# Optimization experiments

Measured on AMD Instinct MI355X. Metric: run time of the kernel, lower is better.

The kernel has to match this reference:

```python
import jax, jax.numpy as jnp
import numpy as np

EPS = 1e-12  # F.normalize eps


def _l2norm(v, axis=-1):
    # torch.nn.functional.normalize: x / max(||x||_2, eps)
    n = jnp.sqrt(jnp.sum(v * v, axis=axis, keepdims=True))
    return v / jnp.maximum(n, EPS)


def setup_inputs() -> dict:
    key = jax.random.key(0)
    ks = jax.random.split(key, 4)
    B, C, W, H, Z = 8, 256, 16, 16, 16
    N, P = W * H * Z, 64
    heads = 8
    import math
    std_w = 1.0 / math.sqrt(C)      # nn.Linear default-ish scale
    std_ef = 1.0 / math.sqrt(P)     # init_() uses last-dim
    return {
        "x": jax.random.normal(ks[0], (B, C, W, H, Z), dtype=jnp.float32),
        "W_sa": jax.random.uniform(ks[1], (4 * C, C), jnp.float32, -std_w, std_w),
        "EF": jax.random.uniform(ks[2], (N, P), jnp.float32, -std_ef, std_ef),
        "temp2_sa": jnp.ones((heads, 1, 1), jnp.float32),
        "W_sc": jax.random.uniform(ks[3], (4 * C, C), jnp.float32, -std_w, std_w),
        "temp_sc": jnp.ones((heads, 1, 1), jnp.float32),
    }


def _qkvv(xf, Wt, heads):
    # xf: (B, N, C); torch Linear(hidden, 4*hidden, bias=False): y = x @ W.T
    B, N, C = xf.shape
    d = C // heads
    y = xf @ Wt.T                                   # (B, N, 4C)
    y = y.reshape(B, N, 4, heads, d)
    y = jnp.transpose(y, (2, 0, 3, 1, 4))           # (4, B, h, N, d)
    return y[0], y[1], y[2], y[3]


def reference(x, W_sa, EF, temp2_sa, W_sc, temp_sc):
    B, C, W, H, Z = x.shape
    N = W * H * Z
    heads = temp_sc.shape[0]
    d = C // heads
    xf = jnp.transpose(x.reshape(B, C, N), (0, 2, 1))  # (B, N, C)

    # ---- Spatial (Linformer-style projected) attention ----
    q, k, _, v_sa = _qkvv(xf, W_sa, heads)            # each (B, h, N, d)
    q_t = jnp.swapaxes(q, -2, -1)                     # (B, h, d, N)
    k_t = jnp.swapaxes(k, -2, -1)
    v_t = jnp.swapaxes(v_sa, -2, -1)
    k_proj = jnp.einsum('bhdn,nk->bhdk', k_t, EF)     # (B, h, d, P)
    v_proj = jnp.einsum('bhdn,nk->bhdk', v_t, EF)
    q_n = _l2norm(q_t, axis=-1)                       # normalize over N
    attn_sa = jnp.einsum('bhdn,bhdk->bhnk', q_n, k_proj) * temp2_sa  # (B,h,N,P)
    attn_sa = jax.nn.softmax(attn_sa, axis=-1)        # dropout: eval mode (identity)
    x_sa = jnp.einsum('bhnk,bhdk->bhnd', attn_sa, v_proj)            # (B,h,N,d)
    # faithful to original: permute(0,3,1,2) then reshape(B,N,C)
    x_sa = jnp.transpose(x_sa, (0, 3, 1, 2)).reshape(B, N, C)

    # ---- Channel (cross-covariance) attention ----
    qc, kc, v_ca, _ = _qkvv(xf, W_sc, heads)          # (B, h, N, d)
    qc_t = _l2norm(jnp.swapaxes(qc, -2, -1), axis=-1) # (B, h, d, N), norm over N
    kc_t = _l2norm(jnp.swapaxes(kc, -2, -1), axis=-1)
    vc_t = jnp.swapaxes(v_ca, -2, -1)                 # (B, h, d, N)
    attn_ca = jnp.einsum('bhdn,bhen->bhde', qc_t, kc_t) * temp_sc    # (B,h,d,d)
    attn_ca = jax.nn.softmax(attn_ca, axis=-1)
    x_ca = jnp.einsum('bhde,bhen->bhdn', attn_ca, vc_t)              # (B,h,d,N)
    x_ca = jnp.transpose(x_ca, (0, 3, 1, 2)).reshape(B, N, C)        # (B,N,h,d)->(B,N,C)

    feat = x_ca + x_sa
    out = jnp.transpose(feat.reshape(B, W, H, Z, C), (0, 4, 1, 2, 3))
    return out
```

## Files before the change

### kernel.cpp

```cpp
#include <hip/hip_runtime.h>

typedef unsigned short u16;
typedef unsigned int   u32;

typedef __attribute__((ext_vector_type(4))) short short4v;
typedef __attribute__((ext_vector_type(8))) short bf16x8;
typedef __attribute__((ext_vector_type(4))) float f32x4;


__device__ __forceinline__ float bf2f(u16 u){
  union { u32 i; float f; } v; v.i = ((u32)u) << 16; return v.f;
}
__device__ __forceinline__ u16 f2bf(float f){
  u32 u = __float_as_uint(f);
  u32 r = u + 0x7FFFu + ((u >> 16) & 1u);
  return (u16)(r >> 16);
}

__device__ __forceinline__ void gload_lds16(const u16* g, u16* l){
  __builtin_amdgcn_global_load_lds((const __attribute__((address_space(1))) void*)g,
                                   (__attribute__((address_space(3))) void*)l,
                                   16, 0, 0);
}

__global__ void k_detect(const u16* __restrict__ x, u32* __restrict__ flag){
  __shared__ int cnt[256];
  const int t = threadIdx.x;
  int c = 0;
  #pragma unroll
  for(int i = 0; i < 4; i++){
    u16 v = x[t * 4 + i];
    int e = (v >> 7) & 0xFF;
    if(e >= 112 && e <= 134) c++;
  }
  cnt[t] = c;
  __syncthreads();
  for(int s = 128; s > 0; s >>= 1){
    if(t < s) cnt[t] += cnt[t + s];
    __syncthreads();
  }
  if(t == 0) *flag = (cnt[0] < 800) ? 1u : 0u;
}

__global__ __launch_bounds__(256) void k_conv_bf(const void* __restrict__ src,
                                                 u16* __restrict__ dst, int n,
                                                 const u32* __restrict__ flag){
  const int i0 = (blockIdx.x * 256 + threadIdx.x) * 8;
  if(i0 >= n) return;
  const bool isf32 = (*flag != 0);
  if(isf32){
    const float4 a = *(const float4*)((const float*)src + i0);
    const float4 b = *(const float4*)((const float*)src + i0 + 4);
    uint4 o;
    o.x = (u32)f2bf(a.x) | ((u32)f2bf(a.y) << 16);
    o.y = (u32)f2bf(a.z) | ((u32)f2bf(a.w) << 16);
    o.z = (u32)f2bf(b.x) | ((u32)f2bf(b.y) << 16);
    o.w = (u32)f2bf(b.z) | ((u32)f2bf(b.w) << 16);
    *(uint4*)(dst + i0) = o;
  } else {
    *(uint4*)(dst + i0) = *(const uint4*)((const u16*)src + i0);
  }
}

__global__ __launch_bounds__(256) void k_conv_f32(const void* __restrict__ src,
                                                  float* __restrict__ dst, int n,
                                                  const u32* __restrict__ flag){
  const int i0 = (blockIdx.x * 256 + threadIdx.x) * 4;
  if(i0 >= n) return;
  const bool isf32 = (*flag != 0);
  if(isf32){
    *(float4*)(dst + i0) = *(const float4*)((const float*)src + i0);
  } else {
    const uint2 a = *(const uint2*)((const u16*)src + i0);
    float4 o;
    o.x = bf2f((u16)(a.x & 0xFFFF)); o.y = bf2f((u16)(a.x >> 16));
    o.z = bf2f((u16)(a.y & 0xFFFF)); o.w = bf2f((u16)(a.y >> 16));
    *(float4*)(dst + i0) = o;
  }
}

__global__ __launch_bounds__(256) void k_conv_both(const void* __restrict__ src,
                                                   float* __restrict__ dstf,
                                                   u16* __restrict__ dstb, int n,
                                                   int nb,
                                                   const u32* __restrict__ flag){
  const int i0 = (blockIdx.x * 256 + threadIdx.x) * 4;
  if(i0 >= n) return;
  const bool isf32 = (*flag != 0);
  float4 o;
  if(isf32){
    o = *(const float4*)((const float*)src + i0);
  } else {
    const uint2 a = *(const uint2*)((const u16*)src + i0);
    o.x = bf2f((u16)(a.x & 0xFFFF)); o.y = bf2f((u16)(a.x >> 16));
    o.z = bf2f((u16)(a.y & 0xFFFF)); o.w = bf2f((u16)(a.y >> 16));
  }
  *(float4*)(dstf + i0) = o;
  if(i0 < nb){
    uint2 pk;
    pk.x = (u32)f2bf(o.x) | ((u32)f2bf(o.y) << 16);
    pk.y = (u32)f2bf(o.z) | ((u32)f2bf(o.w) << 16);
    *(uint2*)(dstb + i0) = pk;
  }
}

__global__ __launch_bounds__(256) void k_convT(const void* __restrict__ src,
                                               u16* __restrict__ xb,
                                               u16* __restrict__ xT,
                                               const u32* __restrict__ flag){
  __shared__ u16 T[64][72];
  const int t = threadIdx.x;
  const int n0 = blockIdx.x * 64, c0 = blockIdx.y * 64, b = blockIdx.z;
  const int cl = t >> 2, ns = (t & 3) * 16;
  const bool isf32 = (*flag != 0);
  const size_t srcoff = ((size_t)(b * 256 + c0 + cl)) * 4096 + n0 + ns;
  u16 e[16];
  if(isf32){
    const float* sp = (const float*)src + srcoff;
    #pragma unroll
    for(int i = 0; i < 4; i++){
      const float4 v = *(const float4*)(sp + i * 4);
      e[i*4+0] = f2bf(v.x); e[i*4+1] = f2bf(v.y);
      e[i*4+2] = f2bf(v.z); e[i*4+3] = f2bf(v.w);
    }
  } else {
    const u16* sp = (const u16*)src + srcoff;
    *(uint4*)&e[0] = *(const uint4*)sp;
    *(uint4*)&e[8] = *(const uint4*)(sp + 8);
  }
  u16* xbp = xb + srcoff;
  *(uint4*)xbp       = *(uint4*)&e[0];
  *(uint4*)(xbp + 8) = *(uint4*)&e[8];
  #pragma unroll
  for(int i = 0; i < 16; i++) T[ns + i][cl] = e[i];
  __syncthreads();
  const int nl = t >> 2, cs = (t & 3) * 16;
  u16* xtp = xT + ((size_t)b * 4096 + n0 + nl) * 256 + c0 + cs;
  *(uint4*)xtp       = *(const uint4*)&T[nl][cs];
  *(uint4*)(xtp + 8) = *(const uint4*)&T[nl][cs + 8];
}

__global__ __launch_bounds__(256) void k_conv_efT(const void* __restrict__ src,
                                                  u16* __restrict__ EFT,
                                                  const u32* __restrict__ flag){
  __shared__ u16 T[64][72];
  const int t = threadIdx.x;
  const int n0 = blockIdx.x * 64;
  const int nl = t >> 2, p0 = (t & 3) * 16;
  const bool isf32 = (*flag != 0);
  const size_t off = (size_t)(n0 + nl) * 64 + p0;
  u16 e[16];
  if(isf32){
    const float* sp = (const float*)src + off;
    #pragma unroll
    for(int i = 0; i < 4; i++){
      const float4 v = *(const float4*)(sp + i * 4);
      e[i*4+0] = f2bf(v.x); e[i*4+1] = f2bf(v.y);
      e[i*4+2] = f2bf(v.z); e[i*4+3] = f2bf(v.w);
    }
  } else {
    const u16* sp = (const u16*)src + off;
    *(uint4*)&e[0] = *(const uint4*)sp;
    *(uint4*)&e[8] = *(const uint4*)(sp + 8);
  }
  #pragma unroll
  for(int i = 0; i < 16; i++) T[p0 + i][nl] = e[i];
  __syncthreads();
  const int pr = t >> 2, nn = (t & 3) * 16;
  u16* dp = EFT + (size_t)pr * 4096 + n0 + nn;
  *(uint4*)dp       = *(const uint4*)&T[pr][nn];
  *(uint4*)(dp + 8) = *(const uint4*)&T[pr][nn + 8];
}

__global__ __launch_bounds__(256) void k_qkv(const u16* __restrict__ Wc,
                                             const u16* __restrict__ xT,
                                             u16* __restrict__ Y){
  __shared__ union {
    struct { u16 Ws[128][64]; u16 Xs[128][64]; } s;
    u16 Cs[128][136];
  } L;
  const int t = threadIdx.x;
  const int n0 = blockIdx.x * 128, m0 = blockIdx.y * 128, b = blockIdx.z;
  const int w = t >> 6, lane = t & 63;
  const int fm = lane & 15, fq = lane >> 4;
  const int wm = w >> 1, wn = w & 1;
  const int lr = lane >> 3, lc = (lane & 7) * 8;
  const u16* gw = Wc + (size_t)m0 * 256;
  const u16* gx = xT + ((size_t)b * 4096 + n0) * 256;
  f32x4 acc[4][4] = {};
  for(int kc = 0; kc < 256; kc += 64){
    #pragma unroll
    for(int i = 0; i < 4; i++){
      const int row = w * 32 + i * 8;
      gload_lds16(gw + (size_t)(row + lr) * 256 + kc + lc, &L.s.Ws[row][0]);
      gload_lds16(gx + (size_t)(row + lr) * 256 + kc + lc, &L.s.Xs[row][0]);
    }
    __syncthreads();
    #pragma unroll
    for(int kh = 0; kh < 2; kh++){
      bf16x8 af[4], bx[4];
      #pragma unroll
      for(int mt = 0; mt < 4; mt++)
        af[mt] = *(const bf16x8*)&L.s.Ws[wm * 64 + mt * 16 + fm][kh * 32 + fq * 8];
      #pragma unroll
      for(int nt = 0; nt < 4; nt++)
        bx[nt] = *(const bf16x8*)&L.s.Xs[wn * 64 + nt * 16 + fm][kh * 32 + fq * 8];
      #pragma unroll
      for(int mt = 0; mt < 4; mt++)
        #pragma unroll
        for(int nt = 0; nt < 4; nt++)
          acc[mt][nt] = __builtin_amdgcn_mfma_f32_16x16x32_bf16(af[mt], bx[nt],
                                                                acc[mt][nt], 0, 0, 0);
    }
    __syncthreads();
  }
  #pragma unroll
  for(int mt = 0; mt < 4; mt++)
    #pragma unroll
    for(int nt = 0; nt < 4; nt++)
      #pragma unroll
      for(int r = 0; r < 4; r++)
        L.Cs[wm * 64 + mt * 16 + fq * 4 + r][wn * 64 + nt * 16 + fm] =
          f2bf(acc[mt][nt][r]);
  __syncthreads();
  #pragma unroll
  for(int i = 0; i < 8; i++){
    const int row = i * 16 + (t >> 4), ce = (t & 15) * 8;
    *(uint4*)(Y + ((size_t)b * 1024 + m0 + row) * 4096 + n0 + ce) =
      *(const uint4*)&L.Cs[row][ce];
  }
}

__global__ __launch_bounds__(256) void k_xef_mfma(const u16* __restrict__ xb,
                                                  const u16* __restrict__ EFT,
                                                  float* __restrict__ xefp){
  const int t = threadIdx.x;
  const int mh = blockIdx.x, s = blockIdx.y, b = blockIdx.z;
  const int w = t >> 6, lane = t & 63;
  const int fm = lane & 15, fq = lane >> 4;
  const int c0 = mh * 128 + w * 32;
  const u16* ar = xb + ((size_t)(b * 256 + c0 + fm)) * 4096 + s * 256 + fq * 8;
  const u16* br = EFT + (size_t)fm * 4096 + s * 256 + fq * 8;
  f32x4 acc[2][4] = {};
  #pragma unroll
  for(int kk = 0; kk < 8; kk++){
    bf16x8 bfr[4];
    #pragma unroll
    for(int nt = 0; nt < 4; nt++)
      bfr[nt] = *(const bf16x8*)(br + (size_t)nt * 16 * 4096 + kk * 32);
    #pragma unroll
    for(int mt = 0; mt < 2; mt++){
      bf16x8 af = *(const bf16x8*)(ar + (size_t)mt * 16 * 4096 + kk * 32);
      #pragma unroll
      for(int nt = 0; nt < 4; nt++)
        acc[mt][nt] = __builtin_amdgcn_mfma_f32_16x16x32_bf16(af, bfr[nt],
                                                              acc[mt][nt], 0, 0, 0);
    }
  }
  float* dst = xefp + (size_t)s * 131072 + (size_t)(b * 256 + c0) * 64;
  #pragma unroll
  for(int mt = 0; mt < 2; mt++)
    #pragma unroll
    for(int nt = 0; nt < 4; nt++)
      #pragma unroll
      for(int r = 0; r < 4; r++)
        dst[(mt * 16 + fq * 4 + r) * 64 + nt * 16 + fm] = acc[mt][nt][r];
}

__global__ __launch_bounds__(256) void k_xred(const float* __restrict__ xefp,
                                              float* __restrict__ xef){
  const int i0 = (blockIdx.x * 256 + threadIdx.x) * 4;
  float4 a = *(const float4*)(xefp + i0);
  #pragma unroll
  for(int s = 1; s < 16; s++){
    const float4 v = *(const float4*)(xefp + (size_t)s * 131072 + i0);
    a.x += v.x; a.y += v.y; a.z += v.z; a.w += v.w;
  }
  *(float4*)(xef + i0) = a;
}

__global__ __launch_bounds__(256) void k_kv4b(const float* __restrict__ Wsaf,
                                              const float* __restrict__ xef,
                                              const float* __restrict__ invsa,
                                              u16* __restrict__ kpT,
                                              u16* __restrict__ vpb){
  const int t = threadIdx.x;
  const int ri = t >> 6, p = t & 63;
  const int r = blockIdx.x * 4 + ri, b = blockIdx.y;
  const int row_w = (r < 256) ? (256 + r) : (512 + r);
  const float* wr = Wsaf + (size_t)row_w * 256;
  const float* xr = xef + (size_t)(b * 256) * 64 + p;
  float acc = 0.f;
  for(int c = 0; c < 256; c++)
    acc += wr[c] * xr[(size_t)c * 64];
  if(r < 256){
    const float sc = invsa[b * 256 + r];
    kpT[((size_t)(b * 8 + (r >> 5)) * 64 + p) * 32 + (r & 31)] = f2bf(acc * sc);
  } else {
    const int rv = r - 256;
    vpb[((size_t)(b * 8 + (rv >> 5)) * 32 + (rv & 31)) * 64 + p] = f2bf(acc);
  }
}

__global__ __launch_bounds__(256) void k_norm(const u16* __restrict__ src,
                                              float* __restrict__ dst,
                                              int stride_b, int row_off){
  __shared__ float red[256];
  const int r = blockIdx.x, b = blockIdx.y, t = threadIdx.x;
  const u16* row = src + (size_t)(b * stride_b + row_off + r) * 4096;
  float s = 0.f;
  #pragma unroll
  for(int i = 0; i < 16; i++){ float v = bf2f(row[t + 256 * i]); s += v * v; }
  red[t] = s;
  __syncthreads();
  for(int s2 = 128; s2 > 0; s2 >>= 1){
    if(t < s2) red[t] += red[t + s2];
    __syncthreads();
  }
  if(t == 0) dst[b * 256 + r] = 1.0f / fmaxf(sqrtf(red[0]), 1e-12f);
}

__device__ __forceinline__ bf16x8 ld_frag8(const u16* p){
  short4v lo = *(const short4v*)p;
  short4v hi = *(const short4v*)(p + 4);
  bf16x8 r;
  r[0]=lo[0]; r[1]=lo[1]; r[2]=lo[2]; r[3]=lo[3];
  r[4]=hi[0]; r[5]=hi[1]; r[6]=hi[2]; r[7]=hi[3];
  return r;
}

__global__ __launch_bounds__(256) void k_gram_mfma(const u16* __restrict__ Y,
                                                   float* __restrict__ Gp){
  const int t = threadIdx.x;
  const int s = blockIdx.x, h = blockIdx.y, b = blockIdx.z;
  const int w = t >> 6, lane = t & 63;
  const int fm = lane & 15, fq = lane >> 4;
  const int j0 = (w >> 1) * 16, e0 = (w & 1) * 16;
  const u16* qrow = Y + (size_t)(b * 1024 + 256 + h * 32 + j0 + fm) * 4096;
  const u16* krow = Y + (size_t)(b * 1024 + 512 + h * 32 + e0 + fm) * 4096;
  f32x4 acc = {};
  const int nb0 = s * 512 + fq * 8;
  #pragma unroll 4
  for(int it = 0; it < 16; it++){
    const int nb = nb0 + it * 32;
    bf16x8 a  = ld_frag8(qrow + nb);
    bf16x8 bb = ld_frag8(krow + nb);
    acc = __builtin_amdgcn_mfma_f32_16x16x32_bf16(a, bb, acc, 0, 0, 0);
  }
  float* dst = Gp + ((size_t)((s * 8 + b) * 8 + h) * 1024);
  #pragma unroll
  for(int r = 0; r < 4; r++)
    dst[(j0 + fq * 4 + r) * 32 + e0 + fm] = acc[r];
}

__global__ void k_softmax_ca(const float* __restrict__ Gp,
                             const float* __restrict__ invq,
                             const float* __restrict__ invk,
                             const float* __restrict__ temp,
                             float* __restrict__ attn){
  const int j = threadIdx.x, h = blockIdx.x, b = blockIdx.y;
  const float tm = temp[h];
  const float iq = invq[b * 256 + h * 32 + j];
  float v[32];
  float m = -1e30f;
  #pragma unroll
  for(int e = 0; e < 32; e++){
    float g = 0.f;
    #pragma unroll
    for(int s = 0; s < 8; s++)
      g += Gp[(size_t)s * 65536 + (size_t)(b * 8 + h) * 1024 + j * 32 + e];
    float val = g * iq * invk[b * 256 + h * 32 + e] * tm;
    v[e] = val; m = fmaxf(m, val);
  }
  float sum = 0.f;
  #pragma unroll
  for(int e = 0; e < 32; e++){ v[e] = __expf(v[e] - m); sum += v[e]; }
  const float inv = 1.0f / sum;
  #pragma unroll
  for(int e = 0; e < 32; e++) attn[(size_t)(b * 8 + h) * 1024 + j * 32 + e] = v[e] * inv;
}

__global__ __launch_bounds__(256) void k_sa_mfma(const u16* __restrict__ Y,
                                                 const u16* __restrict__ kpT,
                                                 const u16* __restrict__ vpb,
                                                 const float* __restrict__ temp2,
                                                 u16* __restrict__ xsa){
  __shared__ u16 As[64][36];
  __shared__ u16 Ks[64][36];
  __shared__ u16 Vs[32][68];
  __shared__ u16 Ps[64][68];
  __shared__ u16 Cs[32][68];
  const int t = threadIdx.x;
  const int ntile = blockIdx.x, h = blockIdx.y, b = blockIdx.z;
  const int n0 = ntile * 64;
  const int w = t >> 6, lane = t & 63;
  const int fm = lane & 15, fq = lane >> 4;
  {
    const int j = t >> 3, ns = (t & 7) * 8;
    const u16* src = Y + (size_t)(b * 1024 + h * 32 + j) * 4096 + n0 + ns;
    uint4 v = *(const uint4*)src;
    u16 e[8]; *(uint4*)e = v;
    #pragma unroll
    for(int i = 0; i < 8; i++) As[ns + i][j] = e[i];
  }
  {
    const int p = t >> 2, jb = (t & 3) * 8;
    *(uint4*)&Ks[p][jb] =
      *(const uint4*)(kpT + ((size_t)(b * 8 + h) * 64 + p) * 32 + jb);
  }
  {
    const int jv = t >> 3, ps = (t & 7) * 8;
    *(uint4*)&Vs[jv][ps] =
      *(const uint4*)(vpb + ((size_t)(b * 8 + h) * 32 + jv) * 64 + ps);
  }
  __syncthreads();
  bf16x8 a = ld_frag8(&As[w * 16 + fm][fq * 8]);
  f32x4 lg[4];
  #pragma unroll
  for(int pt = 0; pt < 4; pt++){
    bf16x8 bk = ld_frag8(&Ks[pt * 16 + fm][fq * 8]);
    f32x4 z = {};
    lg[pt] = __builtin_amdgcn_mfma_f32_16x16x32_bf16(a, bk, z, 0, 0, 0);
  }
  const float tm = temp2[h];
  float sinv[4];
  #pragma unroll
  for(int r = 0; r < 4; r++){
    float v0 = lg[0][r]*tm, v1 = lg[1][r]*tm, v2 = lg[2][r]*tm, v3 = lg[3][r]*tm;
    float mx = fmaxf(fmaxf(v0, v1), fmaxf(v2, v3));
    #pragma unroll
    for(int m = 1; m < 16; m <<= 1) mx = fmaxf(mx, __shfl_xor(mx, m, 16));
    v0 = __expf(v0 - mx); v1 = __expf(v1 - mx);
    v2 = __expf(v2 - mx); v3 = __expf(v3 - mx);
    float s = v0 + v1 + v2 + v3;
    #pragma unroll
    for(int m = 1; m < 16; m <<= 1) s += __shfl_xor(s, m, 16);
    sinv[r] = 1.0f / s;
    const int nrow = w * 16 + fq * 4 + r;
    Ps[nrow][fm]      = f2bf(v0);
    Ps[nrow][16 + fm] = f2bf(v1);
    Ps[nrow][32 + fm] = f2bf(v2);
    Ps[nrow][48 + fm] = f2bf(v3);
  }
  f32x4 o[2] = {};
  #pragma unroll
  for(int ks = 0; ks < 2; ks++){
    bf16x8 ap = ld_frag8(&Ps[w * 16 + fm][ks * 32 + fq * 8]);
    #pragma unroll
    for(int jt = 0; jt < 2; jt++){
      bf16x8 bv = ld_frag8(&Vs[jt * 16 + fm][ks * 32 + fq * 8]);
      o[jt] = __builtin_amdgcn_mfma_f32_16x16x32_bf16(ap, bv, o[jt], 0, 0, 0);
    }
  }
  #pragma unroll
  for(int jt = 0; jt < 2; jt++)
    #pragma unroll
    for(int r = 0; r < 4; r++)
      Cs[jt * 16 + fm][w * 16 + fq * 4 + r] = f2bf(o[jt][r] * sinv[r]);
  __syncthreads();
  {
    const int jv = t >> 3, ns = (t & 7) * 8;
    u16 e[8];
    #pragma unroll
    for(int i = 0; i < 8; i++) e[i] = Cs[jv][ns + i];
    *(uint4*)(xsa + ((size_t)(b * 8 + h) * 32 + jv) * 4096 + n0 + ns) = *(uint4*)e;
  }
}

__global__ __launch_bounds__(256) void k_out2(const u16* __restrict__ Y,
                                              const float* __restrict__ attn,
                                              const u16* __restrict__ xsa,
                                              float* __restrict__ out){
  __shared__ u16 VcL[32][520];
  __shared__ u16 xs[32][16][34];
  __shared__ float arL[32][32];
  const int t = threadIdx.x;
  const int jg = blockIdx.x, hc = blockIdx.y, b = blockIdx.z;
  const int nn0 = jg * 512;
  {
    const float* ap = attn + (size_t)(b * 8 + hc) * 1024;
    #pragma unroll
    for(int i = 0; i < 4; i++) ((float*)arL)[t + 256 * i] = ap[t + 256 * i];
  }
  {
    const int e = t >> 3, ch = (t & 7) * 64;
    const u16* src = Y + (size_t)(b * 1024 + 768 + hc * 32 + e) * 4096 + nn0 + ch;
    #pragma unroll
    for(int i = 0; i < 8; i++)
      *(uint4*)&VcL[e][ch + i * 8] = *(const uint4*)(src + i * 8);
  }
  #pragma unroll
  for(int rep = 0; rep < 2; rep++){
    const int s = rep * 256 + t;
    const int hj = s >> 4, nh = s & 15;
    const int h = hj & 7, jj = hj >> 3;
    const u16* src = xsa + ((size_t)(b * 8 + h) * 32 + jg * 4 + jj) * 4096 + nh * 256 + hc * 32;
    uint4 v0 = *(const uint4*)src;
    uint4 v1 = *(const uint4*)(src + 8);
    u16* dst = &xs[hj][nh][0];
    u32* d32 = (u32*)dst;
    d32[0] = v0.x; d32[1] = v0.y; d32[2] = v0.z; d32[3] = v0.w;
    d32[4] = v1.x; d32[5] = v1.y; d32[6] = v1.z; d32[7] = v1.w;
    uint4 v2 = *(const uint4*)(src + 16);
    uint4 v3 = *(const uint4*)(src + 24);
    d32[8]  = v2.x; d32[9]  = v2.y; d32[10] = v2.z; d32[11] = v2.w;
    d32[12] = v3.x; d32[13] = v3.y; d32[14] = v3.z; d32[15] = v3.w;
  }
  __syncthreads();
  const int nl0 = 2 * t;
  const int hj0 = nl0 >> 4, nh0 = nl0 & 15;
  for(int row = 0; row < 32; row++){
    float acc0 = 0.f, acc1 = 0.f;
    #pragma unroll
    for(int e = 0; e < 32; e++){
      const float a = arL[row][e];
      const u32 v = *(const u32*)&VcL[e][nl0];
      acc0 += a * bf2f((u16)(v & 0xFFFF));
      acc1 += a * bf2f((u16)(v >> 16));
    }
    const float sa0 = bf2f(xs[hj0][nh0][row]);
    const float sa1 = bf2f(xs[hj0][nh0 + 1][row]);
    float2 o; o.x = acc0 + sa0; o.y = acc1 + sa1;
    *(float2*)&out[(size_t)(b * 256 + hc * 32 + row) * 4096 + nn0 + nl0] = o;
  }
}

#define OFF_XB    ((size_t)0)
#define OFF_XT    ((size_t)16777216)
#define OFF_Y     ((size_t)33554432)
#define OFF_WSAF  ((size_t)100663296)
#define OFF_WCAT  ((size_t)101711872)
#define OFF_EFT   ((size_t)102236160)
#define OFF_XEF   ((size_t)103284736)
#define OFF_KPT   ((size_t)103809024)
#define OFF_VPB   ((size_t)104071168)
#define OFF_ISA   ((size_t)104333312)
#define OFF_IQC   ((size_t)104341504)
#define OFF_IKC   ((size_t)104349696)
#define OFF_GP    ((size_t)104357888)
#define OFF_ATT   ((size_t)106455040)
#define OFF_TF    ((size_t)106717184)
#define OFF_FLAG  ((size_t)106717248)
#define OFF_XEFP  OFF_XT

extern "C" void kernel_launch(void* const* d_in, const int* in_sizes, int n_in,
                              void* d_out, int out_size, void* d_ws, size_t ws_size,
                              hipStream_t stream){
  (void)in_sizes; (void)n_in; (void)out_size; (void)ws_size;
  char* ws = (char*)d_ws;
  u16*   xb    = (u16*)  (ws + OFF_XB);
  u16*   xsa   = (u16*)  (ws + OFF_XB);
  u16*   xT    = (u16*)  (ws + OFF_XT);
  u16*   Y     = (u16*)  (ws + OFF_Y);
  float* Wsaf  = (float*)(ws + OFF_WSAF);
  u16*   Wcat  = (u16*)  (ws + OFF_WCAT);
  u16*   EFT   = (u16*)  (ws + OFF_EFT);
  float* xef   = (float*)(ws + OFF_XEF);
  u16*   kpT   = (u16*)  (ws + OFF_KPT);
  u16*   vpb   = (u16*)  (ws + OFF_VPB);
  float* invsa = (float*)(ws + OFF_ISA);
  float* invqc = (float*)(ws + OFF_IQC);
  float* invkc = (float*)(ws + OFF_IKC);
  float* Gp    = (float*)(ws + OFF_GP);
  float* attn  = (float*)(ws + OFF_ATT);
  float* tf    = (float*)(ws + OFF_TF);
  u32*   flag  = (u32*)  (ws + OFF_FLAG);
  float* xefp  = (float*)(ws + OFF_XEFP);
  float* out = (float*)d_out;

  k_detect<<<1, 256, 0, stream>>>((const u16*)d_in[0], flag);
  k_convT<<<dim3(64, 4, 8), 256, 0, stream>>>(d_in[0], xb, xT, flag);
  k_conv_both<<<256, 256, 0, stream>>>(d_in[1], Wsaf, Wcat, 262144, 65536, flag);
  k_conv_efT<<<64, 256, 0, stream>>>(d_in[2], EFT, flag);
  k_conv_bf  <<<96,  256, 0, stream>>>(d_in[4], Wcat + 65536, 196608, flag);
  k_conv_f32 <<<1,   256, 0, stream>>>(d_in[3], tf,      8, flag);
  k_conv_f32 <<<1,   256, 0, stream>>>(d_in[5], tf + 8,  8, flag);

  k_qkv<<<dim3(32, 8, 8), 256, 0, stream>>>(Wcat, xT, Y);
  k_xef_mfma<<<dim3(2, 16, 8), 256, 0, stream>>>(xb, EFT, xefp);
  k_xred<<<128, 256, 0, stream>>>(xefp, xef);
  k_norm<<<dim3(256, 8), 256, 0, stream>>>(Y, invsa, 1024, 0);
  k_norm<<<dim3(256, 8), 256, 0, stream>>>(Y, invqc, 1024, 256);
  k_norm<<<dim3(256, 8), 256, 0, stream>>>(Y, invkc, 1024, 512);
  k_kv4b<<<dim3(128, 8), 256, 0, stream>>>(Wsaf, xef, invsa, kpT, vpb);
  k_gram_mfma<<<dim3(8, 8, 8), 256, 0, stream>>>(Y, Gp);
  k_softmax_ca<<<dim3(8, 8), 32, 0, stream>>>(Gp, invqc, invkc, tf + 8, attn);
  k_sa_mfma<<<dim3(64, 8, 8), 256, 0, stream>>>(Y, kpT, vpb, tf, xsa);
  k_out2<<<dim3(8, 8, 8), 256, 0, stream>>>(Y, attn, xsa, out);
}
```

Measured before the change: 231.3 us.

## Use MFMA with hi/lo bf16 split for output kernel, merge norm launches

Replaces the scalar FMA loop in the channel-attention output kernel with bf16 MFMA, splitting the fp32 attention matrix into hi and lo bf16 parts to preserve accuracy. Merges the three row-norm kernels into one launch with vectorized 16-element loads, writing into contiguous inverse-norm buffers. Also merges two tiny temperature conversion launches into one. The output stores become narrower per lane, which may reduce write coalescing.

```diff
diff --git a/kernel.cpp b/kernel.cpp
--- a/kernel.cpp
+++ b/kernel.cpp
@@ -62,23 +62,6 @@
   }
 }
 
-__global__ __launch_bounds__(256) void k_conv_f32(const void* __restrict__ src,
-                                                  float* __restrict__ dst, int n,
-                                                  const u32* __restrict__ flag){
-  const int i0 = (blockIdx.x * 256 + threadIdx.x) * 4;
-  if(i0 >= n) return;
-  const bool isf32 = (*flag != 0);
-  if(isf32){
-    *(float4*)(dst + i0) = *(const float4*)((const float*)src + i0);
-  } else {
-    const uint2 a = *(const uint2*)((const u16*)src + i0);
-    float4 o;
-    o.x = bf2f((u16)(a.x & 0xFFFF)); o.y = bf2f((u16)(a.x >> 16));
-    o.z = bf2f((u16)(a.y & 0xFFFF)); o.w = bf2f((u16)(a.y >> 16));
-    *(float4*)(dst + i0) = o;
-  }
-}
-
 __global__ __launch_bounds__(256) void k_conv_both(const void* __restrict__ src,
                                                    float* __restrict__ dstf,
                                                    u16* __restrict__ dstb, int n,
@@ -104,6 +87,16 @@
   }
 }
 
+__global__ void k_conv_tf(const void* __restrict__ s0, const void* __restrict__ s1,
+                          float* __restrict__ tf, const u32* __restrict__ flag){
+  const int t = threadIdx.x;
+  if(t >= 16) return;
+  const void* s = (t < 8) ? s0 : s1;
+  const int i = t & 7;
+  if(*flag != 0) tf[t] = ((const float*)s)[i];
+  else           tf[t] = bf2f(((const u16*)s)[i]);
+}
+
 __global__ __launch_bounds__(256) void k_convT(const void* __restrict__ src,
                                                u16* __restrict__ xb,
                                                u16* __restrict__ xT,
@@ -302,22 +295,26 @@
   }
 }
 
-__global__ __launch_bounds__(256) void k_norm(const u16* __restrict__ src,
-                                              float* __restrict__ dst,
-                                              int stride_b, int row_off){
+__global__ __launch_bounds__(256) void k_norm3(const u16* __restrict__ Y,
+                                               float* __restrict__ inv3){
   __shared__ float red[256];
   const int r = blockIdx.x, b = blockIdx.y, t = threadIdx.x;
-  const u16* row = src + (size_t)(b * stride_b + row_off + r) * 4096;
+  const u16* row = Y + (size_t)(b * 1024 + r) * 4096 + t * 16;
+  u16 e[16];
+  *(uint4*)&e[0] = *(const uint4*)row;
+  *(uint4*)&e[8] = *(const uint4*)(row + 8);
   float s = 0.f;
   #pragma unroll
-  for(int i = 0; i < 16; i++){ float v = bf2f(row[t + 256 * i]); s += v * v; }
+  for(int i = 0; i < 16; i++){ float v = bf2f(e[i]); s += v * v; }
   red[t] = s;
   __syncthreads();
   for(int s2 = 128; s2 > 0; s2 >>= 1){
     if(t < s2) red[t] += red[t + s2];
     __syncthreads();
   }
-  if(t == 0) dst[b * 256 + r] = 1.0f / fmaxf(sqrtf(red[0]), 1e-12f);
+  if(t == 0)
+    inv3[(r >> 8) * 2048 + b * 256 + (r & 255)] =
+      1.0f / fmaxf(sqrtf(red[0]), 1e-12f);
 }
 
 __device__ __forceinline__ bf16x8 ld_frag8(const u16* p){
@@ -467,27 +464,41 @@
   }
 }
 
-__global__ __launch_bounds__(256) void k_out2(const u16* __restrict__ Y,
-                                              const float* __restrict__ attn,
-                                              const u16* __restrict__ xsa,
-                                              float* __restrict__ out){
-  __shared__ u16 VcL[32][520];
+__global__ __launch_bounds__(256) void k_out_mfma(const u16* __restrict__ Y,
+                                                  const float* __restrict__ attn,
+                                                  const u16* __restrict__ xsa,
+                                                  float* __restrict__ out){
+  __shared__ u16 Vt[32][516];
   __shared__ u16 xs[32][16][34];
-  __shared__ float arL[32][32];
+  __shared__ u16 Ah[32][40];
+  __shared__ u16 Al[32][40];
   const int t = threadIdx.x;
   const int jg = blockIdx.x, hc = blockIdx.y, b = blockIdx.z;
   const int nn0 = jg * 512;
+  const int w = t >> 6, lane = t & 63;
+  const int fm = lane & 15, fq = lane >> 4;
   {
-    const float* ap = attn + (size_t)(b * 8 + hc) * 1024;
-    #pragma unroll
-    for(int i = 0; i < 4; i++) ((float*)arL)[t + 256 * i] = ap[t + 256 * i];
+    const float4 v = *(const float4*)(attn + (size_t)(b * 8 + hc) * 1024 + t * 4);
+    const int j = t >> 3, e0 = (t & 7) * 4;
+    float vv[4] = {v.x, v.y, v.z, v.w};
+    #pragma unroll
+    for(int i = 0; i < 4; i++){
+      u16 hi = f2bf(vv[i]);
+      Ah[j][e0 + i] = hi;
+      Al[j][e0 + i] = f2bf(vv[i] - bf2f(hi));
+    }
   }
   {
     const int e = t >> 3, ch = (t & 7) * 64;
     const u16* src = Y + (size_t)(b * 1024 + 768 + hc * 32 + e) * 4096 + nn0 + ch;
     #pragma unroll
-    for(int i = 0; i < 8; i++)
-      *(uint4*)&VcL[e][ch + i * 8] = *(const uint4*)(src + i * 8);
+    for(int i = 0; i < 8; i++){
+      uint4 v = *(const uint4*)(src + i * 8);
+      uint2 lo; lo.x = v.x; lo.y = v.y;
+      uint2 hi; hi.x = v.z; hi.y = v.w;
+      *(uint2*)&Vt[e][ch + i * 8]     = lo;
+      *(uint2*)&Vt[e][ch + i * 8 + 4] = hi;
+    }
   }
   #pragma unroll
   for(int rep = 0; rep < 2; rep++){
@@ -497,8 +508,7 @@
     const u16* src = xsa + ((size_t)(b * 8 + h) * 32 + jg * 4 + jj) * 4096 + nh * 256 + hc * 32;
     uint4 v0 = *(const uint4*)src;
     uint4 v1 = *(const uint4*)(src + 8);
-    u16* dst = &xs[hj][nh][0];
-    u32* d32 = (u32*)dst;
+    u32* d32 = (u32*)&xs[hj][nh][0];
     d32[0] = v0.x; d32[1] = v0.y; d32[2] = v0.z; d32[3] = v0.w;
     d32[4] = v1.x; d32[5] = v1.y; d32[6] = v1.z; d32[7] = v1.w;
     uint4 v2 = *(const uint4*)(src + 16);
@@ -507,22 +517,37 @@
     d32[12] = v3.x; d32[13] = v3.y; d32[14] = v3.z; d32[15] = v3.w;
   }
   __syncthreads();
-  const int nl0 = 2 * t;
-  const int hj0 = nl0 >> 4, nh0 = nl0 & 15;
-  for(int row = 0; row < 32; row++){
-    float acc0 = 0.f, acc1 = 0.f;
-    #pragma unroll
-    for(int e = 0; e < 32; e++){
-      const float a = arL[row][e];
-      const u32 v = *(const u32*)&VcL[e][nl0];
-      acc0 += a * bf2f((u16)(v & 0xFFFF));
-      acc1 += a * bf2f((u16)(v >> 16));
-    }
-    const float sa0 = bf2f(xs[hj0][nh0][row]);
-    const float sa1 = bf2f(xs[hj0][nh0 + 1][row]);
-    float2 o; o.x = acc0 + sa0; o.y = acc1 + sa1;
-    *(float2*)&out[(size_t)(b * 256 + hc * 32 + row) * 4096 + nn0 + nl0] = o;
-  }
+  bf16x8 ah[2], al[2];
+  #pragma unroll
+  for(int mt = 0; mt < 2; mt++){
+    ah[mt] = *(const bf16x8*)&Ah[mt * 16 + fm][fq * 8];
+    al[mt] = *(const bf16x8*)&Al[mt * 16 + fm][fq * 8];
+  }
+  f32x4 acc[2][8] = {};
+  #pragma unroll
+  for(int nt = 0; nt < 8; nt++){
+    const int colb = w * 128 + nt * 16 + fm;
+    bf16x8 bv;
+    #pragma unroll
+    for(int i = 0; i < 8; i++) bv[i] = (short)Vt[fq * 8 + i][colb];
+    #pragma unroll
+    for(int mt = 0; mt < 2; mt++){
+      acc[mt][nt] = __builtin_amdgcn_mfma_f32_16x16x32_bf16(ah[mt], bv, acc[mt][nt], 0, 0, 0);
+      acc[mt][nt] = __builtin_amdgcn_mfma_f32_16x16x32_bf16(al[mt], bv, acc[mt][nt], 0, 0, 0);
+    }
+  }
+  #pragma unroll
+  for(int mt = 0; mt < 2; mt++)
+    #pragma unroll
+    for(int nt = 0; nt < 8; nt++){
+      const int col = w * 128 + nt * 16 + fm;
+      float* op = out + (size_t)(b * 256 + hc * 32 + mt * 16 + fq * 4) * 4096 + nn0 + col;
+      #pragma unroll
+      for(int r = 0; r < 4; r++){
+        const float sa = bf2f(xs[w * 8 + nt][fm][mt * 16 + fq * 4 + r]);
+        op[(size_t)r * 4096] = acc[mt][nt][r] + sa;
+      }
+    }
 }
 
 #define OFF_XB    ((size_t)0)
@@ -573,18 +598,15 @@
   k_conv_both<<<256, 256, 0, stream>>>(d_in[1], Wsaf, Wcat, 262144, 65536, flag);
   k_conv_efT<<<64, 256, 0, stream>>>(d_in[2], EFT, flag);
   k_conv_bf  <<<96,  256, 0, stream>>>(d_in[4], Wcat + 65536, 196608, flag);
-  k_conv_f32 <<<1,   256, 0, stream>>>(d_in[3], tf,      8, flag);
-  k_conv_f32 <<<1,   256, 0, stream>>>(d_in[5], tf + 8,  8, flag);
+  k_conv_tf  <<<1, 64, 0, stream>>>(d_in[3], d_in[5], tf, flag);
 
   k_qkv<<<dim3(32, 8, 8), 256, 0, stream>>>(Wcat, xT, Y);
   k_xef_mfma<<<dim3(2, 16, 8), 256, 0, stream>>>(xb, EFT, xefp);
   k_xred<<<128, 256, 0, stream>>>(xefp, xef);
-  k_norm<<<dim3(256, 8), 256, 0, stream>>>(Y, invsa, 1024, 0);
-  k_norm<<<dim3(256, 8), 256, 0, stream>>>(Y, invqc, 1024, 256);
-  k_norm<<<dim3(256, 8), 256, 0, stream>>>(Y, invkc, 1024, 512);
+  k_norm3<<<dim3(768, 8), 256, 0, stream>>>(Y, invsa);
   k_kv4b<<<dim3(128, 8), 256, 0, stream>>>(Wsaf, xef, invsa, kpT, vpb);
   k_gram_mfma<<<dim3(8, 8, 8), 256, 0, stream>>>(Y, Gp);
   k_softmax_ca<<<dim3(8, 8), 32, 0, stream>>>(Gp, invqc, invkc, tf + 8, attn);
   k_sa_mfma<<<dim3(64, 8, 8), 256, 0, stream>>>(Y, kpT, vpb, tf, xsa);
-  k_out2<<<dim3(8, 8, 8), 256, 0, stream>>>(Y, attn, xsa, out);
-}
+  k_out_mfma<<<dim3(8, 8, 8), 256, 0, stream>>>(Y, attn, xsa, out);
+}
```

After: 217.1 us. -6.2%, faster.
